# Optimization experiments

Hardware: AMD Instinct MI355X
Metric: run time of the kernel (lower is better)

The kernel has to match this reference:

```python
import jax, jax.numpy as jnp
import numpy as np

B, S, D, H = 2, 2048, 512, 8
HD = D // H
EPS = 1e-5


def _ln(x, g, b):
    mu = jnp.mean(x, axis=-1, keepdims=True)
    var = jnp.mean((x - mu) ** 2, axis=-1, keepdims=True)
    return (x - mu) * jax.lax.rsqrt(var + EPS) * g + b


def setup_inputs() -> dict:
    key = jax.random.key(0)
    ks = jax.random.split(key, 16)
    x = jax.random.normal(ks[0], (B, S, D), dtype=jnp.float32)
    adj = jax.random.randint(ks[1], (B, S, S), 0, 2, dtype=jnp.int32)
    adj = adj.at[:, jnp.arange(S), jnp.arange(S)].set(1)  # self-loops, avoid all-masked rows
    edge_attr = jax.random.normal(ks[2], (B, S, S), dtype=jnp.float32)
    sc = 1.0 / np.sqrt(D)
    p = lambda k, shp: jax.random.normal(k, shp, dtype=jnp.float32) * sc
    return {
        "x": x, "adj_matrix": adj, "edge_attr_matrix": edge_attr,
        "ln1_g": jnp.ones((D,)), "ln1_b": jnp.zeros((D,)),
        "ln2_g": jnp.ones((D,)), "ln2_b": jnp.zeros((D,)),
        "wq": p(ks[3], (D, D)), "bq": jnp.zeros((D,)),
        "wk": p(ks[4], (D, D)), "bk": jnp.zeros((D,)),
        "wv": p(ks[5], (D, D)), "bv": jnp.zeros((D,)),
        "wo": p(ks[6], (D, D)), "bo": jnp.zeros((D,)),
        "w1": p(ks[7], (D, 4 * D)), "b1": jnp.zeros((4 * D,)),
        "w2": p(ks[8], (4 * D, D)), "b2": jnp.zeros((D,)),
    }


def reference(x, adj_matrix, edge_attr_matrix, ln1_g, ln1_b, ln2_g, ln2_b,
              wq, bq, wk, bk, wv, bv, wo, bo, w1, b1, w2, b2):
    b, s, d = x.shape
    residual = x
    nx = _ln(x, ln1_g, ln1_b)
    q = (nx @ wq + bq).reshape(b, s, H, HD).transpose(0, 2, 1, 3)  # [B,H,S,HD]
    k = (nx @ wk + bk).reshape(b, s, H, HD).transpose(0, 2, 1, 3)
    v = (nx @ wv + bv).reshape(b, s, H, HD).transpose(0, 2, 1, 3)
    adjf = adj_matrix.astype(jnp.float32)
    # bias: -inf where no edge, else 0.1*edge_attr*adj (faithful to score_mod)
    bias = jnp.where(adj_matrix > 0, 0.1 * edge_attr_matrix * adjf, -jnp.inf)[:, None]  # [B,1,S,S]
    scores = jnp.einsum('bhqd,bhkd->bhqk', q, k) / np.sqrt(HD) + bias
    attn = jax.nn.softmax(scores, axis=-1)
    out = jnp.einsum('bhqk,bhkd->bhqd', attn, v)
    out = out.transpose(0, 2, 1, 3).reshape(b, s, d)
    x1 = residual + (out @ wo + bo)
    n2 = _ln(x1, ln2_g, ln2_b)
    mlp = jax.nn.gelu(n2 @ w1 + b1, approximate=False) @ w2 + b2
    return x1 + mlp
```

## Files before the change

### kernel.cpp

```cpp
#include <hip/hip_runtime.h>
#include <cstdint>
#include <cstddef>

typedef __bf16 bf16x8 __attribute__((ext_vector_type(8)));
typedef float f32x4 __attribute__((ext_vector_type(4)));
typedef const __attribute__((address_space(1))) void* gas_t;
typedef __attribute__((address_space(3))) void* las_t;

#define QSCALE 0.18033688011112042f
#define BSCALE 0.14426950408889634f

__device__ __forceinline__ unsigned short f2bf(float f) {
  union { float f; unsigned u; } v; v.f = f;
  unsigned r = v.u + 0x7FFFu + ((v.u >> 16) & 1u);
  return (unsigned short)(r >> 16);
}
__device__ __forceinline__ unsigned short f2bf_fast(float f) {
  union { float f; unsigned u; } v; v.f = f;
  return (unsigned short)((v.u + 0x8000u) >> 16);
}
__device__ __forceinline__ float bf2f(unsigned short h) {
  union { unsigned u; float f; } v; v.u = ((unsigned)h) << 16;
  return v.f;
}
__device__ __forceinline__ void gll16(const void* g, void* l) {
  __builtin_amdgcn_global_load_lds((gas_t)g, (las_t)l, 16, 0, 0);
}

__global__ __launch_bounds__(256) void transpose_cast(const float* __restrict__ in,
                                                      unsigned short* __restrict__ out,
                                                      int R, int C) {
  __shared__ float tile[32][33];
  int bx = blockIdx.x * 32, by = blockIdx.y * 32;
  int tx = threadIdx.x & 31, tg = threadIdx.x >> 5;
  #pragma unroll
  for (int i = 0; i < 4; i++) {
    int r = tg * 4 + i;
    tile[r][tx] = in[(size_t)(by + r) * C + bx + tx];
  }
  __syncthreads();
  #pragma unroll
  for (int i = 0; i < 4; i++) {
    int r = tg * 4 + i;
    out[(size_t)(bx + r) * R + by + tx] = f2bf(tile[tx][r]);
  }
}

struct TP4 { const float* in[4]; unsigned short* out[4]; };
__global__ __launch_bounds__(256) void transpose_cast4(TP4 p) {
  __shared__ float tile[32][33];
  const float* in = p.in[blockIdx.z];
  unsigned short* out = p.out[blockIdx.z];
  int bx = blockIdx.x * 32, by = blockIdx.y * 32;
  int tx = threadIdx.x & 31, tg = threadIdx.x >> 5;
  #pragma unroll
  for (int i = 0; i < 4; i++) {
    int r = tg * 4 + i;
    tile[r][tx] = in[(size_t)(by + r) * 512 + bx + tx];
  }
  __syncthreads();
  #pragma unroll
  for (int i = 0; i < 4; i++) {
    int r = tg * 4 + i;
    out[(size_t)(bx + r) * 512 + by + tx] = f2bf(tile[tx][r]);
  }
}

__global__ __launch_bounds__(256) void bias_pack(const int* __restrict__ adj,
                                                 const float* __restrict__ edge,
                                                 unsigned short* __restrict__ bp) {
  size_t i = ((size_t)blockIdx.x * 256 + threadIdx.x) * 4;
  int4 a = *(const int4*)(adj + i);
  float4 e = *(const float4*)(edge + i);
  ushort4 r;
  r.x = a.x > 0 ? f2bf(BSCALE * e.x * (float)a.x - 20.0f) : f2bf(-30000.0f);
  r.y = a.y > 0 ? f2bf(BSCALE * e.y * (float)a.y - 20.0f) : f2bf(-30000.0f);
  r.z = a.z > 0 ? f2bf(BSCALE * e.z * (float)a.z - 20.0f) : f2bf(-30000.0f);
  r.w = a.w > 0 ? f2bf(BSCALE * e.w * (float)a.w - 20.0f) : f2bf(-30000.0f);
  *(ushort4*)(bp + i) = r;
}

__global__ __launch_bounds__(256) void ln_kernel(const float* __restrict__ x,
                                                 const float* __restrict__ g,
                                                 const float* __restrict__ bt,
                                                 unsigned short* __restrict__ out) {
  int row = blockIdx.x, tid = threadIdx.x;
  float2 v = *(const float2*)(x + (size_t)row * 512 + tid * 2);
  float s = v.x + v.y, s2 = v.x * v.x + v.y * v.y;
  #pragma unroll
  for (int m = 1; m < 64; m <<= 1) { s += __shfl_xor(s, m, 64); s2 += __shfl_xor(s2, m, 64); }
  __shared__ float red[8];
  int w = tid >> 6;
  if ((tid & 63) == 0) { red[w * 2] = s; red[w * 2 + 1] = s2; }
  __syncthreads();
  float ts = red[0] + red[2] + red[4] + red[6];
  float ts2 = red[1] + red[3] + red[5] + red[7];
  float mu = ts * (1.0f / 512.0f);
  float rs = rsqrtf(ts2 * (1.0f / 512.0f) - mu * mu + 1e-5f);
  int c = tid * 2;
  ushort2 o;
  o.x = f2bf((v.x - mu) * rs * g[c] + bt[c]);
  o.y = f2bf((v.y - mu) * rs * g[c + 1] + bt[c + 1]);
  *(ushort2*)(out + (size_t)row * 512 + c) = o;
}

__global__ __launch_bounds__(256) void ln_fuse2(const float* __restrict__ x,
                                                const unsigned short* __restrict__ opp,
                                                const float* __restrict__ bo,
                                                const float* __restrict__ g,
                                                const float* __restrict__ bt,
                                                float* __restrict__ x1,
                                                unsigned short* __restrict__ n2) {
  const size_t MN = (size_t)4096 * 512;
  int row = blockIdx.x, tid = threadIdx.x;
  int c = tid * 2;
  size_t idx = (size_t)row * 512 + c;
  float2 xv = *(const float2*)(x + idx);
  ushort2 p0 = *(const ushort2*)(opp + idx);
  ushort2 p1 = *(const ushort2*)(opp + MN + idx);
  float2 v;
  v.x = xv.x + bo[c]     + bf2f(p0.x) + bf2f(p1.x);
  v.y = xv.y + bo[c + 1] + bf2f(p0.y) + bf2f(p1.y);
  float s = v.x + v.y, s2 = v.x * v.x + v.y * v.y;
  #pragma unroll
  for (int m = 1; m < 64; m <<= 1) { s += __shfl_xor(s, m, 64); s2 += __shfl_xor(s2, m, 64); }
  __shared__ float red[8];
  int w = tid >> 6;
  if ((tid & 63) == 0) { red[w * 2] = s; red[w * 2 + 1] = s2; }
  __syncthreads();
  float ts = red[0] + red[2] + red[4] + red[6];
  float ts2 = red[1] + red[3] + red[5] + red[7];
  float mu = ts * (1.0f / 512.0f);
  float rs = rsqrtf(ts2 * (1.0f / 512.0f) - mu * mu + 1e-5f);
  *(float2*)(x1 + idx) = v;
  ushort2 o;
  o.x = f2bf((v.x - mu) * rs * g[c] + bt[c]);
  o.y = f2bf((v.y - mu) * rs * g[c + 1] + bt[c + 1]);
  *(ushort2*)(n2 + idx) = o;
}

__global__ __launch_bounds__(256) void final_combine(const float* __restrict__ x1,
                                                     const float* __restrict__ b2,
                                                     const unsigned short* __restrict__ mp,
                                                     float* __restrict__ out) {
  const size_t MN = (size_t)4096 * 512;
  size_t i = ((size_t)blockIdx.x * 256 + threadIdx.x) * 4;
  float4 xv = *(const float4*)(x1 + i);
  float4 bv = *(const float4*)(b2 + (i & 511));
  float4 a;
  a.x = xv.x + bv.x; a.y = xv.y + bv.y; a.z = xv.z + bv.z; a.w = xv.w + bv.w;
  #pragma unroll
  for (int sp = 0; sp < 4; sp++) {
    ushort4 p = *(const ushort4*)(mp + sp * MN + i);
    a.x += bf2f(p.x); a.y += bf2f(p.y); a.z += bf2f(p.z); a.w += bf2f(p.w);
  }
  *(float4*)(out + i) = a;
}

struct EpiQKV {
  unsigned short *q, *k, *v;
  const float *bq, *bk, *bv;
  __device__ void operator()(int m, int n, float val) const {
    int b = m >> 11, s = m & 2047;
    int which = n >> 9, col = n & 511;
    int h = col >> 6, d = col & 63;
    int bh = b * 8 + h;
    if (which == 0)      q[((size_t)bh * 2048 + s) * 64 + d] = f2bf((val + bq[col]) * QSCALE);
    else if (which == 1) k[((size_t)bh * 2048 + s) * 64 + d] = f2bf(val + bk[col]);
    else                 v[((size_t)bh * 2048 + s) * 64 + d] = f2bf(val + bv[col]);
  }
};
struct EpiPart {
  unsigned short* dst; int ldn;
  __device__ void operator()(int m, int n, float val) const {
    dst[(size_t)blockIdx.z * 4096 * 512 + (size_t)m * ldn + n] = f2bf(val);
  }
};
struct EpiGelu {
  const float* b1; unsigned short* h;
  __device__ void operator()(int m, int n, float val) const {
    float t = val + b1[n];
    float gl = 0.5f * t * (1.0f + erff(t * 0.70710678118654752f));
    h[(size_t)m * 2048 + n] = f2bf(gl);
  }
};

template <typename Epi>
__global__ __launch_bounds__(256) void gemm_bt(const unsigned short* __restrict__ A,
                                               const unsigned short* __restrict__ Bt,
                                               int lda, int ldb, int kchunk, Epi epi) {
  __shared__ unsigned short a_lds[128 * 64];
  __shared__ unsigned short b_lds[128 * 64];
  const int tid = threadIdx.x;
  const int lane = tid & 63;
  const int w = tid >> 6;
  const int l15 = lane & 15, quad = lane >> 4;
  const int wm = w >> 1, wn = w & 1;
  const int m0 = blockIdx.y * 128, n0 = blockIdx.x * 128;
  const int K0 = blockIdx.z * kchunk, K1 = K0 + kchunk;

  f32x4 acc[4][4] = {};

  for (int k0 = K0; k0 < K1; k0 += 64) {
    __syncthreads();
    #pragma unroll
    for (int i = 0; i < 4; i++) {
      int c = tid + i * 256;
      int g = c >> 6;
      int row = (g >> 1) * 16 + l15;
      int col = (g & 1) * 32 + quad * 8;
      gll16(A + (size_t)(m0 + row) * lda + k0 + col, a_lds + (size_t)(c & ~63) * 8);
      gll16(Bt + (size_t)(n0 + row) * ldb + k0 + col, b_lds + (size_t)(c & ~63) * 8);
    }
    __syncthreads();
    bf16x8 af[4][2], bfr[4][2];
    #pragma unroll
    for (int t = 0; t < 4; t++)
      #pragma unroll
      for (int ks = 0; ks < 2; ks++) {
        af[t][ks]  = *(const bf16x8*)(a_lds + (((size_t)(wm * 4 + t) * 2 + ks) * 64 + lane) * 8);
        bfr[t][ks] = *(const bf16x8*)(b_lds + (((size_t)(wn * 4 + t) * 2 + ks) * 64 + lane) * 8);
      }
    #pragma unroll
    for (int mt = 0; mt < 4; mt++)
      #pragma unroll
      for (int nt = 0; nt < 4; nt++) {
        acc[mt][nt] = __builtin_amdgcn_mfma_f32_16x16x32_bf16(af[mt][0], bfr[nt][0], acc[mt][nt], 0, 0, 0);
        acc[mt][nt] = __builtin_amdgcn_mfma_f32_16x16x32_bf16(af[mt][1], bfr[nt][1], acc[mt][nt], 0, 0, 0);
      }
  }
  #pragma unroll
  for (int mt = 0; mt < 4; mt++)
    #pragma unroll
    for (int nt = 0; nt < 4; nt++)
      #pragma unroll
      for (int r = 0; r < 4; r++)
        epi(m0 + wm * 64 + mt * 16 + quad * 4 + r, n0 + wn * 64 + nt * 16 + l15, acc[mt][nt][r]);
}

__global__ __launch_bounds__(256) void vt_kernel(const unsigned short* __restrict__ vb,
                                                 unsigned short* __restrict__ vbT) {
  __shared__ unsigned short tile[64][72];
  const int bh = blockIdx.y, s0 = blockIdx.x * 64;
  const int tid = threadIdx.x;
  const unsigned short* src = vb + ((size_t)bh * 2048 + s0) * 64;
  #pragma unroll
  for (int i = 0; i < 2; i++) {
    int r = (tid >> 3) + i * 32;
    int c8 = (tid & 7) * 8;
    *(uint4*)(&tile[r][c8]) = *(const uint4*)(src + (size_t)r * 64 + c8);
  }
  __syncthreads();
  unsigned short* dst = vbT + (size_t)bh * 64 * 2048 + s0;
  #pragma unroll
  for (int i = 0; i < 2; i++) {
    int d = (tid >> 3) + i * 32;
    int s8 = (tid & 7) * 8;
    ushort4 o0, o1;
    o0.x = tile[s8 + 0][d]; o0.y = tile[s8 + 1][d]; o0.z = tile[s8 + 2][d]; o0.w = tile[s8 + 3][d];
    o1.x = tile[s8 + 4][d]; o1.y = tile[s8 + 5][d]; o1.z = tile[s8 + 6][d]; o1.w = tile[s8 + 7][d];
    *(ushort4*)(dst + (size_t)d * 2048 + s8) = o0;
    *(ushort4*)(dst + (size_t)d * 2048 + s8 + 4) = o1;
  }
}

__global__ __launch_bounds__(256, 4) void attn_kernel(const unsigned short* __restrict__ Q,
                                                      const unsigned short* __restrict__ Kb,
                                                      const unsigned short* __restrict__ VT,
                                                      const unsigned short* __restrict__ biasp,
                                                      unsigned short* __restrict__ o_part,
                                                      float* __restrict__ l_part) {
  __shared__ unsigned short k_lds[64 * 64];
  __shared__ unsigned short v_lds[64 * 64];
  __shared__ unsigned short p_lds[4][2][16 * 72];

  const int tid = threadIdx.x;
  const int lane = tid & 63, w = tid >> 6;
  const int l15 = lane & 15, quad = lane >> 4;
  const int bh = blockIdx.x, b = bh >> 3;
  const int q0 = blockIdx.y * 128;
  const int split = blockIdx.z;

  bf16x8 qf[2][2];
  const unsigned short* brow[2];
  #pragma unroll
  for (int g = 0; g < 2; g++) {
    const unsigned short* qrow = Q + ((size_t)bh * 2048 + q0 + w * 32 + g * 16 + l15) * 64;
    qf[g][0] = *(const bf16x8*)(qrow + quad * 8);
    qf[g][1] = *(const bf16x8*)(qrow + 32 + quad * 8);
    brow[g] = biasp + ((size_t)b * 2048 + q0 + w * 32 + g * 16 + l15) * 2048;
  }

  f32x4 o_acc[2][4] = {};
  float l_acc[2] = {0.0f, 0.0f};

  const unsigned short* kbase = Kb + (size_t)bh * 2048 * 64;
  const unsigned short* vbase = VT + (size_t)bh * 64 * 2048;

  const int kt0 = split * 8, kt1 = kt0 + 8;
  for (int kt = kt0; kt < kt1; kt++) {
    const int kcol0 = kt * 64;
    __syncthreads();
    #pragma unroll
    for (int i = 0; i < 2; i++) {
      int c = tid + i * 256;
      int g = c >> 6;
      int mt = g >> 1, kk = g & 1;
      int rr = mt * 16 + l15;
      int cc = kk * 32 + quad * 8;
      gll16(kbase + (size_t)(kcol0 + rr) * 64 + cc, k_lds + (size_t)(c & ~63) * 8);
      gll16(vbase + (size_t)rr * 2048 + kcol0 + cc, v_lds + (size_t)(c & ~63) * 8);
    }
    ushort4 bl[2][4];
    #pragma unroll
    for (int g = 0; g < 2; g++)
      #pragma unroll
      for (int mt = 0; mt < 4; mt++)
        bl[g][mt] = *(const ushort4*)(brow[g] + kcol0 + mt * 16 + quad * 4);
    __syncthreads();

    #pragma unroll
    for (int mt = 0; mt < 4; mt++) {
      bf16x8 a0 = *(const bf16x8*)(k_lds + ((size_t)(mt * 2 + 0) * 64 + lane) * 8);
      bf16x8 a1 = *(const bf16x8*)(k_lds + ((size_t)(mt * 2 + 1) * 64 + lane) * 8);
      #pragma unroll
      for (int g = 0; g < 2; g++) {
        f32x4 cb;
        cb[0] = bf2f(bl[g][mt].x); cb[1] = bf2f(bl[g][mt].y);
        cb[2] = bf2f(bl[g][mt].z); cb[3] = bf2f(bl[g][mt].w);
        f32x4 accv = __builtin_amdgcn_mfma_f32_16x16x32_bf16(a0, qf[g][0], cb, 0, 0, 0);
        accv = __builtin_amdgcn_mfma_f32_16x16x32_bf16(a1, qf[g][1], accv, 0, 0, 0);
        float p0 = exp2f(accv[0]), p1 = exp2f(accv[1]);
        float p2 = exp2f(accv[2]), p3 = exp2f(accv[3]);
        l_acc[g] += (p0 + p1) + (p2 + p3);
        ushort4 pv;
        pv.x = f2bf_fast(p0); pv.y = f2bf_fast(p1); pv.z = f2bf_fast(p2); pv.w = f2bf_fast(p3);
        *(ushort4*)(p_lds[w][g] + l15 * 72 + mt * 16 + quad * 4) = pv;
      }
    }

    bf16x8 pf[2][2];
    #pragma unroll
    for (int g = 0; g < 2; g++) {
      pf[g][0] = *(const bf16x8*)(p_lds[w][g] + l15 * 72 + quad * 8);
      pf[g][1] = *(const bf16x8*)(p_lds[w][g] + l15 * 72 + 32 + quad * 8);
    }
    #pragma unroll
    for (int dt = 0; dt < 4; dt++) {
      bf16x8 v0 = *(const bf16x8*)(v_lds + ((size_t)(dt * 2 + 0) * 64 + lane) * 8);
      bf16x8 v1 = *(const bf16x8*)(v_lds + ((size_t)(dt * 2 + 1) * 64 + lane) * 8);
      #pragma unroll
      for (int g = 0; g < 2; g++) {
        o_acc[g][dt] = __builtin_amdgcn_mfma_f32_16x16x32_bf16(pf[g][0], v0, o_acc[g][dt], 0, 0, 0);
        o_acc[g][dt] = __builtin_amdgcn_mfma_f32_16x16x32_bf16(pf[g][1], v1, o_acc[g][dt], 0, 0, 0);
      }
    }
  }

  const size_t obase = ((size_t)split * 16 + bh) * 2048;
  #pragma unroll
  for (int g = 0; g < 2; g++) {
    float l = l_acc[g];
    l += __shfl_xor(l, 16, 64);
    l += __shfl_xor(l, 32, 64);
    if (quad == 0) l_part[obase + q0 + w * 32 + g * 16 + l15] = l;
    #pragma unroll
    for (int dt = 0; dt < 4; dt++)
      #pragma unroll
      for (int r = 0; r < 4; r++)
        o_part[(obase + q0 + w * 32 + g * 16 + quad * 4 + r) * 64 + dt * 16 + l15] =
            f2bf(o_acc[g][dt][r]);
  }
}

__global__ __launch_bounds__(256) void combine_kernel(const unsigned short* __restrict__ o_part,
                                                      const float* __restrict__ l_part,
                                                      unsigned short* __restrict__ ao) {
  const int row = blockIdx.x;
  const int b = row >> 11, s = row & 2047;
  const int col = threadIdx.x * 2;
  const int h = col >> 6, d = col & 63;
  const int bh = b * 8 + h;
  float ox = 0.0f, oy = 0.0f, l = 0.0f;
  #pragma unroll
  for (int sp = 0; sp < 4; sp++) {
    size_t base = (size_t)(sp * 16 + bh) * 2048 + s;
    ushort2 o = *(const ushort2*)(o_part + base * 64 + d);
    ox += bf2f(o.x); oy += bf2f(o.y);
    l += l_part[base];
  }
  float inv = 1.0f / l;
  ushort2 o;
  o.x = f2bf(ox * inv);
  o.y = f2bf(oy * inv);
  *(ushort2*)(ao + (size_t)row * 512 + col) = o;
}

extern "C" void kernel_launch(void* const* d_in, const int* in_sizes, int n_in,
                              void* d_out, int out_size, void* d_ws, size_t ws_size,
                              hipStream_t stream) {
  (void)in_sizes; (void)n_in; (void)out_size; (void)ws_size;
  const float* x    = (const float*)d_in[0];
  const int*   adj  = (const int*)d_in[1];
  const float* edge = (const float*)d_in[2];
  const float* ln1g = (const float*)d_in[3];
  const float* ln1b = (const float*)d_in[4];
  const float* ln2g = (const float*)d_in[5];
  const float* ln2b = (const float*)d_in[6];
  const float* wq = (const float*)d_in[7];  const float* bq = (const float*)d_in[8];
  const float* wk = (const float*)d_in[9];  const float* bk = (const float*)d_in[10];
  const float* wv = (const float*)d_in[11]; const float* bv = (const float*)d_in[12];
  const float* wo = (const float*)d_in[13]; const float* bo = (const float*)d_in[14];
  const float* w1 = (const float*)d_in[15]; const float* b1 = (const float*)d_in[16];
  const float* w2 = (const float*)d_in[17]; const float* b2 = (const float*)d_in[18];
  float* out = (float*)d_out;

  char* ws = (char*)d_ws;
  unsigned short* qkvT = (unsigned short*)ws; ws += (size_t)1536 * 512 * 2;
  unsigned short* woT  = (unsigned short*)ws; ws += (size_t)512 * 512 * 2;
  unsigned short* w1T  = (unsigned short*)ws; ws += (size_t)2048 * 512 * 2;
  unsigned short* w2T  = (unsigned short*)ws; ws += (size_t)512 * 2048 * 2;
  unsigned short* bp   = (unsigned short*)ws;
  unsigned short* opp  = (unsigned short*)ws; ws += (size_t)2 * 2048 * 2048 * 2;
  unsigned short* nx   = (unsigned short*)ws;
  unsigned short* n2   = (unsigned short*)ws; ws += (size_t)4096 * 512 * 2;
  unsigned short* qb   = (unsigned short*)ws;
  unsigned short* ao   = (unsigned short*)ws; ws += (size_t)4096 * 512 * 2;
  unsigned short* kb   = (unsigned short*)ws; ws += (size_t)4096 * 512 * 2;
  unsigned short* vb   = (unsigned short*)ws;
  float*          x1   = (float*)ws;          ws += (size_t)4096 * 512 * 2;
  unsigned short* vbT  = (unsigned short*)ws; ws += (size_t)4096 * 512 * 2;
  char* region1 = ws;
  unsigned short* opt  = (unsigned short*)region1;
  unsigned short* hb   = (unsigned short*)region1;
  float*          lpt  = (float*)(region1 + (size_t)4 * 16 * 2048 * 64 * 2);
  unsigned short* mp   = (unsigned short*)(region1 + (size_t)4 * 16 * 2048 * 64 * 2);

  dim3 blk(256);
  TP4 tp; tp.in[0] = wq; tp.in[1] = wk; tp.in[2] = wv; tp.in[3] = wo;
  tp.out[0] = qkvT; tp.out[1] = qkvT + (size_t)512 * 512;
  tp.out[2] = qkvT + (size_t)2 * 512 * 512; tp.out[3] = woT;
  transpose_cast4<<<dim3(16, 16, 4), blk, 0, stream>>>(tp);
  transpose_cast<<<dim3(64, 16), blk, 0, stream>>>(w1, w1T, 512, 2048);
  transpose_cast<<<dim3(16, 64), blk, 0, stream>>>(w2, w2T, 2048, 512);
  bias_pack<<<8192, blk, 0, stream>>>(adj, edge, bp);
  ln_kernel<<<4096, blk, 0, stream>>>(x, ln1g, ln1b, nx);
  gemm_bt<<<dim3(12, 32, 1), blk, 0, stream>>>(nx, qkvT, 512, 512, 512,
                                               EpiQKV{qb, kb, vb, bq, bk, bv});
  vt_kernel<<<dim3(32, 16), blk, 0, stream>>>(vb, vbT);
  attn_kernel<<<dim3(16, 16, 4), blk, 0, stream>>>(qb, kb, vbT, bp, opt, lpt);
  combine_kernel<<<4096, blk, 0, stream>>>(opt, lpt, ao);
  gemm_bt<<<dim3(4, 32, 2), blk, 0, stream>>>(ao, woT, 512, 512, 256,
                                              EpiPart{opp, 512});
  ln_fuse2<<<4096, blk, 0, stream>>>(x, opp, bo, ln2g, ln2b, x1, n2);
  gemm_bt<<<dim3(16, 32, 1), blk, 0, stream>>>(n2, w1T, 512, 512, 512,
                                               EpiGelu{b1, hb});
  gemm_bt<<<dim3(4, 32, 4), blk, 0, stream>>>(hb, w2T, 2048, 2048, 512,
                                              EpiPart{mp, 512});
  final_combine<<<2048, blk, 0, stream>>>(x1, b2, mp, out);
}
```

Measured before the change: 321.7 us.

## Double-buffer GEMM LDS tiles and make attention LDS-free with register shuffles

The GEMM kernel gets two LDS buffers so the next K tile is fetched while the current one is computed, which removes one barrier per iteration, and its launch bounds now ask for 2 blocks per CU. The attention kernel stops staging K, V and P through shared memory. Each wave loads its K and V fragments straight from global memory and rearranges the packed bf16 probabilities into the P@V operand layout with cross-lane shuffles, so there are no __syncthreads. The catch is redundant global reads of K and V by every wave, plus extra shuffle instructions. The mp workspace pointer is also moved so it no longer overlaps lpt.

```diff
diff --git a/kernel.cpp b/kernel.cpp
--- a/kernel.cpp
+++ b/kernel.cpp
@@ -15,13 +15,13 @@
   unsigned r = v.u + 0x7FFFu + ((v.u >> 16) & 1u);
   return (unsigned short)(r >> 16);
 }
-__device__ __forceinline__ unsigned short f2bf_fast(float f) {
-  union { float f; unsigned u; } v; v.f = f;
-  return (unsigned short)((v.u + 0x8000u) >> 16);
-}
 __device__ __forceinline__ float bf2f(unsigned short h) {
   union { unsigned u; float f; } v; v.u = ((unsigned)h) << 16;
   return v.f;
+}
+__device__ __forceinline__ unsigned pack_bf16(float p0, float p1) {
+  union { float f; unsigned u; } a, b; a.f = p0; b.f = p1;
+  return __builtin_amdgcn_perm(b.u + 0x8000u, a.u + 0x8000u, 0x07060302u);
 }
 __device__ __forceinline__ void gll16(const void* g, void* l) {
   __builtin_amdgcn_global_load_lds((gas_t)g, (las_t)l, 16, 0, 0);
@@ -186,40 +186,54 @@
 };
 
 template <typename Epi>
-__global__ __launch_bounds__(256) void gemm_bt(const unsigned short* __restrict__ A,
-                                               const unsigned short* __restrict__ Bt,
-                                               int lda, int ldb, int kchunk, Epi epi) {
-  __shared__ unsigned short a_lds[128 * 64];
-  __shared__ unsigned short b_lds[128 * 64];
+__global__ __launch_bounds__(256, 2) void gemm_bt(const unsigned short* __restrict__ A,
+                                                  const unsigned short* __restrict__ Bt,
+                                                  int lda, int ldb, int kchunk, Epi epi) {
+  __shared__ unsigned short a_lds[2][128 * 64];
+  __shared__ unsigned short b_lds[2][128 * 64];
   const int tid = threadIdx.x;
   const int lane = tid & 63;
   const int w = tid >> 6;
   const int l15 = lane & 15, quad = lane >> 4;
   const int wm = w >> 1, wn = w & 1;
   const int m0 = blockIdx.y * 128, n0 = blockIdx.x * 128;
-  const int K0 = blockIdx.z * kchunk, K1 = K0 + kchunk;
+  const int K0 = blockIdx.z * kchunk;
+  const int nIter = kchunk >> 6;
 
   f32x4 acc[4][4] = {};
 
-  for (int k0 = K0; k0 < K1; k0 += 64) {
+  #pragma unroll
+  for (int i = 0; i < 4; i++) {
+    int c = tid + i * 256;
+    int g = c >> 6;
+    int row = (g >> 1) * 16 + l15;
+    int col = (g & 1) * 32 + quad * 8;
+    gll16(A + (size_t)(m0 + row) * lda + K0 + col, a_lds[0] + (size_t)(c & ~63) * 8);
+    gll16(Bt + (size_t)(n0 + row) * ldb + K0 + col, b_lds[0] + (size_t)(c & ~63) * 8);
+  }
+
+  for (int it = 0; it < nIter; it++) {
+    const int cur = it & 1;
     __syncthreads();
-    #pragma unroll
-    for (int i = 0; i < 4; i++) {
-      int c = tid + i * 256;
-      int g = c >> 6;
-      int row = (g >> 1) * 16 + l15;
-      int col = (g & 1) * 32 + quad * 8;
-      gll16(A + (size_t)(m0 + row) * lda + k0 + col, a_lds + (size_t)(c & ~63) * 8);
-      gll16(Bt + (size_t)(n0 + row) * ldb + k0 + col, b_lds + (size_t)(c & ~63) * 8);
+    if (it + 1 < nIter) {
+      const int kn = K0 + (it + 1) * 64;
+      #pragma unroll
+      for (int i = 0; i < 4; i++) {
+        int c = tid + i * 256;
+        int g = c >> 6;
+        int row = (g >> 1) * 16 + l15;
+        int col = (g & 1) * 32 + quad * 8;
+        gll16(A + (size_t)(m0 + row) * lda + kn + col, a_lds[1 - cur] + (size_t)(c & ~63) * 8);
+        gll16(Bt + (size_t)(n0 + row) * ldb + kn + col, b_lds[1 - cur] + (size_t)(c & ~63) * 8);
+      }
     }
-    __syncthreads();
     bf16x8 af[4][2], bfr[4][2];
     #pragma unroll
     for (int t = 0; t < 4; t++)
       #pragma unroll
       for (int ks = 0; ks < 2; ks++) {
-        af[t][ks]  = *(const bf16x8*)(a_lds + (((size_t)(wm * 4 + t) * 2 + ks) * 64 + lane) * 8);
-        bfr[t][ks] = *(const bf16x8*)(b_lds + (((size_t)(wn * 4 + t) * 2 + ks) * 64 + lane) * 8);
+        af[t][ks]  = *(const bf16x8*)(a_lds[cur] + (((size_t)(wm * 4 + t) * 2 + ks) * 64 + lane) * 8);
+        bfr[t][ks] = *(const bf16x8*)(b_lds[cur] + (((size_t)(wn * 4 + t) * 2 + ks) * 64 + lane) * 8);
       }
     #pragma unroll
     for (int mt = 0; mt < 4; mt++)
@@ -270,89 +284,84 @@
                                                       const unsigned short* __restrict__ biasp,
                                                       unsigned short* __restrict__ o_part,
                                                       float* __restrict__ l_part) {
-  __shared__ unsigned short k_lds[64 * 64];
-  __shared__ unsigned short v_lds[64 * 64];
-  __shared__ unsigned short p_lds[4][2][16 * 72];
-
   const int tid = threadIdx.x;
   const int lane = tid & 63, w = tid >> 6;
   const int l15 = lane & 15, quad = lane >> 4;
   const int bh = blockIdx.x, b = bh >> 3;
-  const int q0 = blockIdx.y * 128;
+  const int q0 = blockIdx.y * 128 + w * 32;
   const int split = blockIdx.z;
 
   bf16x8 qf[2][2];
   const unsigned short* brow[2];
   #pragma unroll
   for (int g = 0; g < 2; g++) {
-    const unsigned short* qrow = Q + ((size_t)bh * 2048 + q0 + w * 32 + g * 16 + l15) * 64;
+    const unsigned short* qrow = Q + ((size_t)bh * 2048 + q0 + g * 16 + l15) * 64;
     qf[g][0] = *(const bf16x8*)(qrow + quad * 8);
     qf[g][1] = *(const bf16x8*)(qrow + 32 + quad * 8);
-    brow[g] = biasp + ((size_t)b * 2048 + q0 + w * 32 + g * 16 + l15) * 2048;
-  }
+    brow[g] = biasp + ((size_t)b * 2048 + q0 + g * 16 + l15) * 2048;
+  }
+
+  const unsigned short* krow = Kb + ((size_t)bh * 2048 + l15) * 64;
+  const unsigned short* vrow0 = VT + ((size_t)bh * 64 + l15) * 2048;
 
   f32x4 o_acc[2][4] = {};
   float l_acc[2] = {0.0f, 0.0f};
 
-  const unsigned short* kbase = Kb + (size_t)bh * 2048 * 64;
-  const unsigned short* vbase = VT + (size_t)bh * 64 * 2048;
-
-  const int kt0 = split * 8, kt1 = kt0 + 8;
-  for (int kt = kt0; kt < kt1; kt++) {
-    const int kcol0 = kt * 64;
-    __syncthreads();
+  const int srcA = ((lane & 16) << 1) | l15;
+  const int srcB = srcA + 16;
+  const bool hiTile = quad >= 2;
+
+  const int kt0 = split * 8;
+  for (int kt = kt0; kt < kt0 + 8; kt++) {
+    const int kcol = kt * 64;
     #pragma unroll
-    for (int i = 0; i < 2; i++) {
-      int c = tid + i * 256;
-      int g = c >> 6;
-      int mt = g >> 1, kk = g & 1;
-      int rr = mt * 16 + l15;
-      int cc = kk * 32 + quad * 8;
-      gll16(kbase + (size_t)(kcol0 + rr) * 64 + cc, k_lds + (size_t)(c & ~63) * 8);
-      gll16(vbase + (size_t)rr * 2048 + kcol0 + cc, v_lds + (size_t)(c & ~63) * 8);
-    }
-    ushort4 bl[2][4];
-    #pragma unroll
-    for (int g = 0; g < 2; g++)
-      #pragma unroll
-      for (int mt = 0; mt < 4; mt++)
-        bl[g][mt] = *(const ushort4*)(brow[g] + kcol0 + mt * 16 + quad * 4);
-    __syncthreads();
-
-    #pragma unroll
-    for (int mt = 0; mt < 4; mt++) {
-      bf16x8 a0 = *(const bf16x8*)(k_lds + ((size_t)(mt * 2 + 0) * 64 + lane) * 8);
-      bf16x8 a1 = *(const bf16x8*)(k_lds + ((size_t)(mt * 2 + 1) * 64 + lane) * 8);
+    for (int H = 0; H < 2; H++) {
+      bf16x8 kf[2][2];
+      #pragma unroll
+      for (int t = 0; t < 2; t++) {
+        const unsigned short* kp = krow + (size_t)(kcol + (2 * H + t) * 16) * 64;
+        kf[t][0] = *(const bf16x8*)(kp + quad * 8);
+        kf[t][1] = *(const bf16x8*)(kp + 32 + quad * 8);
+      }
+      unsigned pk[2][2][2];
+      #pragma unroll
+      for (int t = 0; t < 2; t++) {
+        const int mt16 = (2 * H + t) * 16;
+        #pragma unroll
+        for (int g = 0; g < 2; g++) {
+          ushort4 bl = *(const ushort4*)(brow[g] + kcol + mt16 + quad * 4);
+          f32x4 cb;
+          cb[0] = bf2f(bl.x); cb[1] = bf2f(bl.y); cb[2] = bf2f(bl.z); cb[3] = bf2f(bl.w);
+          f32x4 s = __builtin_amdgcn_mfma_f32_16x16x32_bf16(kf[t][0], qf[g][0], cb, 0, 0, 0);
+          s = __builtin_amdgcn_mfma_f32_16x16x32_bf16(kf[t][1], qf[g][1], s, 0, 0, 0);
+          float p0 = exp2f(s[0]), p1 = exp2f(s[1]), p2 = exp2f(s[2]), p3 = exp2f(s[3]);
+          l_acc[g] += (p0 + p1) + (p2 + p3);
+          pk[t][g][0] = pack_bf16(p0, p1);
+          pk[t][g][1] = pack_bf16(p2, p3);
+        }
+      }
+      bf16x8 vf[4];
+      #pragma unroll
+      for (int dt = 0; dt < 4; dt++)
+        vf[dt] = *(const bf16x8*)(vrow0 + (size_t)dt * 16 * 2048 + kcol + H * 32 + quad * 8);
       #pragma unroll
       for (int g = 0; g < 2; g++) {
-        f32x4 cb;
-        cb[0] = bf2f(bl[g][mt].x); cb[1] = bf2f(bl[g][mt].y);
-        cb[2] = bf2f(bl[g][mt].z); cb[3] = bf2f(bl[g][mt].w);
-        f32x4 accv = __builtin_amdgcn_mfma_f32_16x16x32_bf16(a0, qf[g][0], cb, 0, 0, 0);
-        accv = __builtin_amdgcn_mfma_f32_16x16x32_bf16(a1, qf[g][1], accv, 0, 0, 0);
-        float p0 = exp2f(accv[0]), p1 = exp2f(accv[1]);
-        float p2 = exp2f(accv[2]), p3 = exp2f(accv[3]);
-        l_acc[g] += (p0 + p1) + (p2 + p3);
-        ushort4 pv;
-        pv.x = f2bf_fast(p0); pv.y = f2bf_fast(p1); pv.z = f2bf_fast(p2); pv.w = f2bf_fast(p3);
-        *(ushort4*)(p_lds[w][g] + l15 * 72 + mt * 16 + quad * 4) = pv;
-      }
-    }
-
-    bf16x8 pf[2][2];
-    #pragma unroll
-    for (int g = 0; g < 2; g++) {
-      pf[g][0] = *(const bf16x8*)(p_lds[w][g] + l15 * 72 + quad * 8);
-      pf[g][1] = *(const bf16x8*)(p_lds[w][g] + l15 * 72 + 32 + quad * 8);
-    }
-    #pragma unroll
-    for (int dt = 0; dt < 4; dt++) {
-      bf16x8 v0 = *(const bf16x8*)(v_lds + ((size_t)(dt * 2 + 0) * 64 + lane) * 8);
-      bf16x8 v1 = *(const bf16x8*)(v_lds + ((size_t)(dt * 2 + 1) * 64 + lane) * 8);
-      #pragma unroll
-      for (int g = 0; g < 2; g++) {
-        o_acc[g][dt] = __builtin_amdgcn_mfma_f32_16x16x32_bf16(pf[g][0], v0, o_acc[g][dt], 0, 0, 0);
-        o_acc[g][dt] = __builtin_amdgcn_mfma_f32_16x16x32_bf16(pf[g][1], v1, o_acc[g][dt], 0, 0, 0);
+        unsigned r0a = (unsigned)__shfl((int)pk[0][g][0], srcA);
+        unsigned r0b = (unsigned)__shfl((int)pk[1][g][0], srcA);
+        unsigned r1a = (unsigned)__shfl((int)pk[0][g][1], srcA);
+        unsigned r1b = (unsigned)__shfl((int)pk[1][g][1], srcA);
+        unsigned r2a = (unsigned)__shfl((int)pk[0][g][0], srcB);
+        unsigned r2b = (unsigned)__shfl((int)pk[1][g][0], srcB);
+        unsigned r3a = (unsigned)__shfl((int)pk[0][g][1], srcB);
+        unsigned r3b = (unsigned)__shfl((int)pk[1][g][1], srcB);
+        union { uint4 u; bf16x8 v; } fr;
+        fr.u.x = hiTile ? r0b : r0a;
+        fr.u.y = hiTile ? r1b : r1a;
+        fr.u.z = hiTile ? r2b : r2a;
+        fr.u.w = hiTile ? r3b : r3a;
+        #pragma unroll
+        for (int dt = 0; dt < 4; dt++)
+          o_acc[g][dt] = __builtin_amdgcn_mfma_f32_16x16x32_bf16(fr.v, vf[dt], o_acc[g][dt], 0, 0, 0);
       }
     }
   }
@@ -363,12 +372,12 @@
     float l = l_acc[g];
     l += __shfl_xor(l, 16, 64);
     l += __shfl_xor(l, 32, 64);
-    if (quad == 0) l_part[obase + q0 + w * 32 + g * 16 + l15] = l;
+    if (quad == 0) l_part[obase + q0 + g * 16 + l15] = l;
     #pragma unroll
     for (int dt = 0; dt < 4; dt++)
       #pragma unroll
       for (int r = 0; r < 4; r++)
-        o_part[(obase + q0 + w * 32 + g * 16 + quad * 4 + r) * 64 + dt * 16 + l15] =
+        o_part[(obase + q0 + g * 16 + quad * 4 + r) * 64 + dt * 16 + l15] =
             f2bf(o_acc[g][dt][r]);
   }
 }
@@ -434,7 +443,7 @@
   unsigned short* opt  = (unsigned short*)region1;
   unsigned short* hb   = (unsigned short*)region1;
   float*          lpt  = (float*)(region1 + (size_t)4 * 16 * 2048 * 64 * 2);
-  unsigned short* mp   = (unsigned short*)(region1 + (size_t)4 * 16 * 2048 * 64 * 2);
+  unsigned short* mp   = (unsigned short*)(region1 + (size_t)4 * 16 * 2048 * 64 * 2 + 524288);
 
   dim3 blk(256);
   TP4 tp; tp.in[0] = wq; tp.in[1] = wk; tp.in[2] = wv; tp.in[3] = wo;
```

Result: slower. 366.4 us (+13.9%).
